# Kernel tuning notes

Measured on AMD Instinct MI355X. Metric: run time of the kernel, lower is better.

## Reference

```python
import jax, jax.numpy as jnp
import numpy as np

B, MENU, N, M = 4096, 256, 8, 16


def setup_inputs() -> dict:
    key = jax.random.key(0)
    k1, k2, k3, k4 = jax.random.split(key, 4)
    input_bids = jax.random.uniform(k1, (B, N, M), dtype=jnp.float32)
    allocs = jax.random.uniform(k2, (B, MENU, N, M), dtype=jnp.float32)
    # bidder weights must be strictly positive (divided by in payments)
    w = jax.random.uniform(k3, (B, N), dtype=jnp.float32, minval=0.5, maxval=1.5)
    b = jax.random.normal(k4, (B, MENU), dtype=jnp.float32)
    softmax_temp = jnp.asarray(100.0, dtype=jnp.float32)
    return {"input_bids": input_bids, "allocs": allocs, "w": w, "b": b,
            "softmax_temp": softmax_temp}


def reference(input_bids, allocs, w, b, softmax_temp):
    Bsz, n, m = input_bids.shape
    # append the "null" menu entry (zero allocation, zero boost)
    allocs = jnp.concatenate([allocs, jnp.zeros((Bsz, 1, n, m), allocs.dtype)], axis=1)  # B,S,n,m
    b = jnp.concatenate([b, jnp.zeros((Bsz, 1), b.dtype)], axis=1)                        # B,S

    # utility of each agent under each menu entry
    util = jnp.einsum('bsnm,bnm->bsn', allocs, input_bids)        # B,S,n
    per_agent_welfare = w[:, None, :] * util                      # B,S,n
    total_welfare = per_agent_welfare.sum(-1)                     # B,S

    alloc_choice = jax.nn.softmax((total_welfare + b) * softmax_temp, axis=-1)  # B,S
    item_allocation = jnp.einsum('bs,bsnm->bnm', alloc_choice, allocs)          # B,n,m
    chosen_welfare = jnp.einsum('bsn,bs->bn', per_agent_welfare, alloc_choice)  # B,n

    # leave-one-out (VCG-style) payments, vectorized over the removed agent i
    mask = 1.0 - jnp.eye(n, dtype=per_agent_welfare.dtype)        # n,n; row i zeros agent i
    removed_welfare = per_agent_welfare[None] * mask[:, None, None, :]  # i,B,S,n
    total_removed = removed_welfare.sum(-1)                       # i,B,S
    removed_choice = jax.nn.softmax((total_removed + b[None]) * softmax_temp, axis=-1)  # i,B,S

    removed_chosen_sum = jnp.einsum('ibsn,ibs->ib', removed_welfare, removed_choice)  # i,B
    masked_chosen_sum = jnp.einsum('bn,in->ib', chosen_welfare, mask)                 # i,B
    removed_b = jnp.einsum('ibs,bs->ib', removed_choice, b)                           # i,B
    alloc_b = jnp.einsum('bs,bs->b', alloc_choice, b)                                 # B

    payments = (removed_chosen_sum + removed_b - masked_chosen_sum - alloc_b[None]) / w.T  # n,B
    return alloc_choice, item_allocation, payments, allocs
```

## Files before the change

### kernel.cpp

```cpp
#include <hip/hip_runtime.h>

#define NAGENTS 8
#define MITEMS 16
#define NM 128
#define MENU 256
#define SFULL 257

__device__ __forceinline__ float wredmax(float v) {
#pragma unroll
    for (int o = 32; o; o >>= 1) v = fmaxf(v, __shfl_xor(v, o));
    return v;
}
__device__ __forceinline__ float wredsum(float v) {
#pragma unroll
    for (int o = 32; o; o >>= 1) v += __shfl_xor(v, o);
    return v;
}

__global__ __launch_bounds__(512, 4) void cama_kernel(
    const float* __restrict__ bids,
    const float* __restrict__ allocs,
    const float* __restrict__ wvec,
    const float* __restrict__ bvec,
    const float* __restrict__ tempp,
    float* __restrict__ out, int Bsz)
{
    __shared__ float4 lda4[128 * 32];
    __shared__ float lds_pwT[NAGENTS * MENU];
    __shared__ float lds_tot[MENU];
    __shared__ float lds_bb[MENU];
    __shared__ __align__(16) float lds_bids[NM];
    __shared__ float lds_w[NAGENTS];
    __shared__ float lds_ch[SFULL];
    __shared__ float lds_rcs[NAGENTS], lds_rb[NAGENTS], lds_cw[NAGENTS];
    __shared__ float lds_ab;

    const int u = threadIdx.x;
    const int lane = u & 63;
    const int wave = u >> 6;
    const int n = u & 7;
    const int sg = u >> 3;
    const int b = blockIdx.x;
    const size_t bb = (size_t)b;

    float* out_choice = out;
    float* out_item   = out + (size_t)Bsz * SFULL;
    float* out_pay    = out_item + (size_t)Bsz * NM;
    float* out_all    = out_pay + (size_t)NAGENTS * Bsz;

    if (u < NM) lds_bids[u] = bids[bb * NM + u];
    if (u >= NM && u < NM + NAGENTS) lds_w[u - NM] = wvec[bb * NAGENTS + (u - NM)];
    if (u >= 256) lds_bb[u - 256] = bvec[bb * MENU + (u - 256)];
    __syncthreads();

    const float temp = tempp[0];
    const float w_n = lds_w[n];
    const float4* bq = (const float4*)lds_bids + (n << 2);
    const float4 q0 = bq[0], q1 = bq[1], q2 = bq[2], q3 = bq[3];

    float4 P00, P01, P02, P03, P10, P11, P12, P13;

#pragma unroll
    for (int c = 0; c < 4; ++c) {
        const int s = (c << 6) + sg;
        const float4* src = (const float4*)(allocs + ((bb << 8) + s) * NM) + (n << 2);
        float4 a0 = src[0], a1 = src[1], a2 = src[2], a3 = src[3];
        float4* dst = (float4*)(out_all + (bb * SFULL + s) * NM) + (n << 2);
        dst[0] = a0; dst[1] = a1; dst[2] = a2; dst[3] = a3;
        float util = a0.x*q0.x + a0.y*q0.y + a0.z*q0.z + a0.w*q0.w
                   + a1.x*q1.x + a1.y*q1.y + a1.z*q1.z + a1.w*q1.w
                   + a2.x*q2.x + a2.y*q2.y + a2.z*q2.z + a2.w*q2.w
                   + a3.x*q3.x + a3.y*q3.y + a3.z*q3.z + a3.w*q3.w;
        float pwv = w_n * util;
        lds_pwT[(n << 8) + (s ^ (n << 2))] = pwv;
        float t4 = pwv;
        t4 += __shfl_xor(t4, 1);
        t4 += __shfl_xor(t4, 2);
        t4 += __shfl_xor(t4, 4);
        if (n == 0) lds_tot[s] = t4;
        if (c == 0)      { P00 = a0; P01 = a1; P02 = a2; P03 = a3; }
        else if (c == 1) { P10 = a0; P11 = a1; P12 = a2; P13 = a3; }
        else {
            const int base = (s - 128) << 5, c7 = s & 7, j0 = n << 2;
            lda4[base + ((j0 + 0) ^ c7)] = a0;
            lda4[base + ((j0 + 1) ^ c7)] = a1;
            lda4[base + ((j0 + 2) ^ c7)] = a2;
            lda4[base + ((j0 + 3) ^ c7)] = a3;
        }
    }
    if (u < 32) {
        float4 z = make_float4(0.f, 0.f, 0.f, 0.f);
        ((float4*)(out_all + (bb * SFULL + MENU) * NM))[u] = z;
    }
    __syncthreads();

    if (wave == 0) {
        float xs[4], bl[4], es[4];
        float mx = -1e30f;
#pragma unroll
        for (int c = 0; c < 4; ++c) {
            int v = (c << 6) | lane;
            bl[c] = lds_bb[v];
            float x = (lds_tot[v] + bl[c]) * temp;
            xs[c] = x; mx = fmaxf(mx, x);
        }
        mx = fmaxf(wredmax(mx), 0.f);
        float se = 0.f, sab = 0.f;
#pragma unroll
        for (int c = 0; c < 4; ++c) { es[c] = __expf(xs[c] - mx); se += es[c]; sab += es[c] * bl[c]; }
        float en = __expf(-mx);
        se = wredsum(se) + en;
        sab = wredsum(sab);
        float inv = 1.f / se;
#pragma unroll
        for (int c = 0; c < 4; ++c) {
            int v = (c << 6) | lane;
            float chv = es[c] * inv;
            lds_ch[v] = chv;
            out_choice[bb * SFULL + v] = chv;
        }
        if (lane == 0) {
            float chn = en * inv;
            lds_ch[MENU] = chn;
            out_choice[bb * SFULL + MENU] = chn;
            lds_ab = sab * inv;
        }
    }
    {
        const int i = wave;
        float xs[4], trs[4], bl[4];
        float mx = -1e30f;
#pragma unroll
        for (int c = 0; c < 4; ++c) {
            int v = (c << 6) | lane;
            bl[c] = lds_bb[v];
            float tr = lds_tot[v] - lds_pwT[(i << 8) + (v ^ (i << 2))];
            trs[c] = tr;
            float x = (tr + bl[c]) * temp;
            xs[c] = x; mx = fmaxf(mx, x);
        }
        mx = fmaxf(wredmax(mx), 0.f);
        float se = 0.f, s1 = 0.f, s2 = 0.f;
#pragma unroll
        for (int c = 0; c < 4; ++c) {
            float e = __expf(xs[c] - mx);
            se += e; s1 += e * trs[c]; s2 += e * bl[c];
        }
        se = wredsum(se) + __expf(-mx);
        s1 = wredsum(s1);
        s2 = wredsum(s2);
        if (lane == 0) { lds_rcs[i] = s1 / se; lds_rb[i] = s2 / se; }
    }
    __syncthreads();

    {
        const int i = wave;
        float cwv = 0.f;
#pragma unroll
        for (int c = 0; c < 4; ++c) {
            int v = (c << 6) | lane;
            cwv += lds_ch[v] * lds_pwT[(i << 8) + (v ^ (i << 2))];
        }
        cwv = wredsum(cwv);
        if (lane == 0) lds_cw[i] = cwv;
    }
    __syncthreads();

    float* scratchA = lds_pwT;
    float* scratchB = lds_pwT + 1024;
    {
        float c0 = lds_ch[sg], c1 = lds_ch[64 + sg];
        float vs[16];
        vs[ 0] = P00.x*c0 + P10.x*c1;  vs[ 1] = P00.y*c0 + P10.y*c1;
        vs[ 2] = P00.z*c0 + P10.z*c1;  vs[ 3] = P00.w*c0 + P10.w*c1;
        vs[ 4] = P01.x*c0 + P11.x*c1;  vs[ 5] = P01.y*c0 + P11.y*c1;
        vs[ 6] = P01.z*c0 + P11.z*c1;  vs[ 7] = P01.w*c0 + P11.w*c1;
        vs[ 8] = P02.x*c0 + P12.x*c1;  vs[ 9] = P02.y*c0 + P12.y*c1;
        vs[10] = P02.z*c0 + P12.z*c1;  vs[11] = P02.w*c0 + P12.w*c1;
        vs[12] = P03.x*c0 + P13.x*c1;  vs[13] = P03.y*c0 + P13.y*c1;
        vs[14] = P03.z*c0 + P13.z*c1;  vs[15] = P03.w*c0 + P13.w*c1;
#pragma unroll
        for (int wd = 0; wd < 16; ++wd) {
            float t = vs[wd];
            t += __shfl_xor(t, 8);
            t += __shfl_xor(t, 16);
            t += __shfl_xor(t, 32);
            vs[wd] = t;
        }
        if (lane < 8) {
            float4* d4 = (float4*)(scratchA + (wave << 7) + (lane << 4));
            d4[0] = make_float4(vs[ 0], vs[ 1], vs[ 2], vs[ 3]);
            d4[1] = make_float4(vs[ 4], vs[ 5], vs[ 6], vs[ 7]);
            d4[2] = make_float4(vs[ 8], vs[ 9], vs[10], vs[11]);
            d4[3] = make_float4(vs[12], vs[13], vs[14], vs[15]);
        }
    }
    {
        const int nm = u & 127, k = u >> 7;
        const int jj = nm >> 2, r = nm & 3;
        const float* ldf = (const float*)lda4;
        float acc = 0.f;
#pragma unroll 8
        for (int it = 0; it < 32; ++it) {
            int sl = (k << 5) + it;
            acc += lds_ch[128 + sl] * ldf[(sl << 7) + (((jj ^ (sl & 7)) << 2) | r)];
        }
        scratchB[(k << 7) + nm] = acc;
    }
    __syncthreads();

    if (u < NM) {
        float sum = 0.f;
#pragma unroll
        for (int w = 0; w < 8; ++w) sum += scratchA[(w << 7) + u];
#pragma unroll
        for (int k = 0; k < 4; ++k) sum += scratchB[(k << 7) + u];
        out_item[bb * NM + u] = sum;
    }
    if (u < NAGENTS) {
        float ctot = 0.f;
#pragma unroll
        for (int k = 0; k < NAGENTS; ++k) ctot += lds_cw[k];
        float pay = (lds_rcs[u] + lds_rb[u] - (ctot - lds_cw[u]) - lds_ab) / lds_w[u];
        out_pay[(size_t)u * Bsz + b] = pay;
    }
}

extern "C" void kernel_launch(void* const* d_in, const int* in_sizes, int n_in,
                              void* d_out, int out_size, void* d_ws, size_t ws_size,
                              hipStream_t stream) {
    const float* bids   = (const float*)d_in[0];
    const float* allocs = (const float*)d_in[1];
    const float* wvec   = (const float*)d_in[2];
    const float* bvec   = (const float*)d_in[3];
    const float* tempp  = (const float*)d_in[4];
    float* out = (float*)d_out;
    const int Bsz = in_sizes[0] / (NAGENTS * MITEMS);
    cama_kernel<<<Bsz, 512, 0, stream>>>(bids, allocs, wvec, bvec, tempp, out, Bsz);
}
```

Before: 255.4 us.

## Keep all alloc rows in registers, drop LDS staging, defer output copy

```diff
diff --git a/kernel.cpp b/kernel.cpp
--- a/kernel.cpp
+++ b/kernel.cpp
@@ -25,13 +25,11 @@
     const float* __restrict__ tempp,
     float* __restrict__ out, int Bsz)
 {
-    __shared__ float4 lda4[128 * 32];
     __shared__ float lds_pwT[NAGENTS * MENU];
     __shared__ float lds_tot[MENU];
     __shared__ float lds_bb[MENU];
-    __shared__ __align__(16) float lds_bids[NM];
-    __shared__ float lds_w[NAGENTS];
     __shared__ float lds_ch[SFULL];
+    __shared__ float lds_scr[8 * NM];
     __shared__ float lds_rcs[NAGENTS], lds_rb[NAGENTS], lds_cw[NAGENTS];
     __shared__ float lds_ab;
 
@@ -48,29 +46,34 @@
     float* out_pay    = out_item + (size_t)Bsz * NM;
     float* out_all    = out_pay + (size_t)NAGENTS * Bsz;
 
-    if (u < NM) lds_bids[u] = bids[bb * NM + u];
-    if (u >= NM && u < NM + NAGENTS) lds_w[u - NM] = wvec[bb * NAGENTS + (u - NM)];
-    if (u >= 256) lds_bb[u - 256] = bvec[bb * MENU + (u - 256)];
-    __syncthreads();
+    if (u < MENU) lds_bb[u] = bvec[bb * MENU + u];
 
     const float temp = tempp[0];
-    const float w_n = lds_w[n];
-    const float4* bq = (const float4*)lds_bids + (n << 2);
-    const float4 q0 = bq[0], q1 = bq[1], q2 = bq[2], q3 = bq[3];
-
-    float4 P00, P01, P02, P03, P10, P11, P12, P13;
+    const float w_n = wvec[bb * NAGENTS + n];
+    float qf[16];
+    {
+        const float4* bq = (const float4*)(bids + bb * NM) + (n << 2);
+        float4 qa = bq[0], qb = bq[1], qc = bq[2], qd = bq[3];
+        qf[0]=qa.x; qf[1]=qa.y; qf[2]=qa.z; qf[3]=qa.w;
+        qf[4]=qb.x; qf[5]=qb.y; qf[6]=qb.z; qf[7]=qb.w;
+        qf[8]=qc.x; qf[9]=qc.y; qf[10]=qc.z; qf[11]=qc.w;
+        qf[12]=qd.x; qf[13]=qd.y; qf[14]=qd.z; qf[15]=qd.w;
+    }
+
+    float Pf[4][16];
 
 #pragma unroll
     for (int c = 0; c < 4; ++c) {
         const int s = (c << 6) + sg;
         const float4* src = (const float4*)(allocs + ((bb << 8) + s) * NM) + (n << 2);
         float4 a0 = src[0], a1 = src[1], a2 = src[2], a3 = src[3];
-        float4* dst = (float4*)(out_all + (bb * SFULL + s) * NM) + (n << 2);
-        dst[0] = a0; dst[1] = a1; dst[2] = a2; dst[3] = a3;
-        float util = a0.x*q0.x + a0.y*q0.y + a0.z*q0.z + a0.w*q0.w
-                   + a1.x*q1.x + a1.y*q1.y + a1.z*q1.z + a1.w*q1.w
-                   + a2.x*q2.x + a2.y*q2.y + a2.z*q2.z + a2.w*q2.w
-                   + a3.x*q3.x + a3.y*q3.y + a3.z*q3.z + a3.w*q3.w;
+        Pf[c][0]=a0.x;  Pf[c][1]=a0.y;  Pf[c][2]=a0.z;  Pf[c][3]=a0.w;
+        Pf[c][4]=a1.x;  Pf[c][5]=a1.y;  Pf[c][6]=a1.z;  Pf[c][7]=a1.w;
+        Pf[c][8]=a2.x;  Pf[c][9]=a2.y;  Pf[c][10]=a2.z; Pf[c][11]=a2.w;
+        Pf[c][12]=a3.x; Pf[c][13]=a3.y; Pf[c][14]=a3.z; Pf[c][15]=a3.w;
+        float util = 0.f;
+#pragma unroll
+        for (int k = 0; k < 16; ++k) util += Pf[c][k] * qf[k];
         float pwv = w_n * util;
         lds_pwT[(n << 8) + (s ^ (n << 2))] = pwv;
         float t4 = pwv;
@@ -78,19 +81,6 @@
         t4 += __shfl_xor(t4, 2);
         t4 += __shfl_xor(t4, 4);
         if (n == 0) lds_tot[s] = t4;
-        if (c == 0)      { P00 = a0; P01 = a1; P02 = a2; P03 = a3; }
-        else if (c == 1) { P10 = a0; P11 = a1; P12 = a2; P13 = a3; }
-        else {
-            const int base = (s - 128) << 5, c7 = s & 7, j0 = n << 2;
-            lda4[base + ((j0 + 0) ^ c7)] = a0;
-            lda4[base + ((j0 + 1) ^ c7)] = a1;
-            lda4[base + ((j0 + 2) ^ c7)] = a2;
-            lda4[base + ((j0 + 3) ^ c7)] = a3;
-        }
-    }
-    if (u < 32) {
-        float4 z = make_float4(0.f, 0.f, 0.f, 0.f);
-        ((float4*)(out_all + (bb * SFULL + MENU) * NM))[u] = z;
     }
     __syncthreads();
 
@@ -113,16 +103,9 @@
         sab = wredsum(sab);
         float inv = 1.f / se;
 #pragma unroll
-        for (int c = 0; c < 4; ++c) {
-            int v = (c << 6) | lane;
-            float chv = es[c] * inv;
-            lds_ch[v] = chv;
-            out_choice[bb * SFULL + v] = chv;
-        }
+        for (int c = 0; c < 4; ++c) lds_ch[(c << 6) | lane] = es[c] * inv;
         if (lane == 0) {
-            float chn = en * inv;
-            lds_ch[MENU] = chn;
-            out_choice[bb * SFULL + MENU] = chn;
+            lds_ch[MENU] = en * inv;
             lds_ab = sab * inv;
         }
     }
@@ -164,64 +147,54 @@
         cwv = wredsum(cwv);
         if (lane == 0) lds_cw[i] = cwv;
     }
-    __syncthreads();
-
-    float* scratchA = lds_pwT;
-    float* scratchB = lds_pwT + 1024;
-    {
-        float c0 = lds_ch[sg], c1 = lds_ch[64 + sg];
+    {
+        const float ch0 = lds_ch[sg], ch1 = lds_ch[64 + sg],
+                    ch2 = lds_ch[128 + sg], ch3 = lds_ch[192 + sg];
         float vs[16];
-        vs[ 0] = P00.x*c0 + P10.x*c1;  vs[ 1] = P00.y*c0 + P10.y*c1;
-        vs[ 2] = P00.z*c0 + P10.z*c1;  vs[ 3] = P00.w*c0 + P10.w*c1;
-        vs[ 4] = P01.x*c0 + P11.x*c1;  vs[ 5] = P01.y*c0 + P11.y*c1;
-        vs[ 6] = P01.z*c0 + P11.z*c1;  vs[ 7] = P01.w*c0 + P11.w*c1;
-        vs[ 8] = P02.x*c0 + P12.x*c1;  vs[ 9] = P02.y*c0 + P12.y*c1;
-        vs[10] = P02.z*c0 + P12.z*c1;  vs[11] = P02.w*c0 + P12.w*c1;
-        vs[12] = P03.x*c0 + P13.x*c1;  vs[13] = P03.y*c0 + P13.y*c1;
-        vs[14] = P03.z*c0 + P13.z*c1;  vs[15] = P03.w*c0 + P13.w*c1;
 #pragma unroll
         for (int wd = 0; wd < 16; ++wd) {
-            float t = vs[wd];
+            float t = Pf[0][wd]*ch0 + Pf[1][wd]*ch1 + Pf[2][wd]*ch2 + Pf[3][wd]*ch3;
             t += __shfl_xor(t, 8);
             t += __shfl_xor(t, 16);
             t += __shfl_xor(t, 32);
             vs[wd] = t;
         }
         if (lane < 8) {
-            float4* d4 = (float4*)(scratchA + (wave << 7) + (lane << 4));
-            d4[0] = make_float4(vs[ 0], vs[ 1], vs[ 2], vs[ 3]);
-            d4[1] = make_float4(vs[ 4], vs[ 5], vs[ 6], vs[ 7]);
-            d4[2] = make_float4(vs[ 8], vs[ 9], vs[10], vs[11]);
+            float4* d4 = (float4*)(lds_scr + (wave << 7) + (lane << 4));
+            d4[0] = make_float4(vs[0],  vs[1],  vs[2],  vs[3]);
+            d4[1] = make_float4(vs[4],  vs[5],  vs[6],  vs[7]);
+            d4[2] = make_float4(vs[8],  vs[9],  vs[10], vs[11]);
             d4[3] = make_float4(vs[12], vs[13], vs[14], vs[15]);
         }
     }
-    {
-        const int nm = u & 127, k = u >> 7;
-        const int jj = nm >> 2, r = nm & 3;
-        const float* ldf = (const float*)lda4;
-        float acc = 0.f;
-#pragma unroll 8
-        for (int it = 0; it < 32; ++it) {
-            int sl = (k << 5) + it;
-            acc += lds_ch[128 + sl] * ldf[(sl << 7) + (((jj ^ (sl & 7)) << 2) | r)];
-        }
-        scratchB[(k << 7) + nm] = acc;
-    }
     __syncthreads();
 
+#pragma unroll
+    for (int c = 0; c < 4; ++c) {
+        const int s = (c << 6) + sg;
+        float4* dst = (float4*)(out_all + (bb * SFULL + s) * NM) + (n << 2);
+        dst[0] = make_float4(Pf[c][0],  Pf[c][1],  Pf[c][2],  Pf[c][3]);
+        dst[1] = make_float4(Pf[c][4],  Pf[c][5],  Pf[c][6],  Pf[c][7]);
+        dst[2] = make_float4(Pf[c][8],  Pf[c][9],  Pf[c][10], Pf[c][11]);
+        dst[3] = make_float4(Pf[c][12], Pf[c][13], Pf[c][14], Pf[c][15]);
+    }
+    if (u < 32) {
+        ((float4*)(out_all + (bb * SFULL + MENU) * NM))[u] =
+            make_float4(0.f, 0.f, 0.f, 0.f);
+    }
+    if (u < SFULL) out_choice[bb * SFULL + u] = lds_ch[u];
     if (u < NM) {
         float sum = 0.f;
 #pragma unroll
-        for (int w = 0; w < 8; ++w) sum += scratchA[(w << 7) + u];
-#pragma unroll
-        for (int k = 0; k < 4; ++k) sum += scratchB[(k << 7) + u];
+        for (int w = 0; w < 8; ++w) sum += lds_scr[(w << 7) + u];
         out_item[bb * NM + u] = sum;
     }
     if (u < NAGENTS) {
         float ctot = 0.f;
 #pragma unroll
         for (int k = 0; k < NAGENTS; ++k) ctot += lds_cw[k];
-        float pay = (lds_rcs[u] + lds_rb[u] - (ctot - lds_cw[u]) - lds_ab) / lds_w[u];
+        float pay = (lds_rcs[u] + lds_rb[u] - (ctot - lds_cw[u]) - lds_ab)
+                    / wvec[bb * NAGENTS + u];
         out_pay[(size_t)u * Bsz + b] = pay;
     }
 }
```

New measurement: 271.3 us. 6.2% more time.
